# Kernel tuning notes

Hardware: AMD Instinct MI355X
Metric: run time of the kernel (lower is better)

## Reference

```python
import jax, jax.numpy as jnp
import numpy as np

D = 512          # feature dim
N = 4095         # context length
LMBD = 0.9       # eligibility-trace decay
DIM = 2 * D + 1  # 1025
CTX = N + 1      # 4096


def make_M(n: int, lmbd: float) -> jnp.ndarray:
    # M[row, col] = lmbd**(row-col) for col <= row < n, col < n; last row and
    # last column are all zero (M[-1, -1] explicitly zeroed in the original).
    i = jnp.arange(n, dtype=jnp.int32)
    diff = i[:, None] - i[None, :]
    core = jnp.where(diff >= 0, jnp.float32(lmbd) ** jnp.maximum(diff, 0).astype(jnp.float32), 0.0)
    M = jnp.zeros((n + 1, n + 1), dtype=jnp.float32)
    return M.at[:n, :n].set(core)


def setup_inputs() -> dict:
    key = jax.random.key(0)
    kz, kp, kq = jax.random.split(key, 3)
    Z = jax.random.normal(kz, (DIM, CTX), dtype=jnp.float32)
    # nn.Parameter(torch.empty(...)) is uninitialized in the source; use small
    # random values as stand-ins for trained parameters.
    P = jax.random.normal(kp, (DIM, DIM), dtype=jnp.float32) * 0.02
    Q = jax.random.normal(kq, (DIM, DIM), dtype=jnp.float32) * 0.02
    M = make_M(N, LMBD)
    return {"Z": Z, "P": P, "Q": Q, "M": M}


def reference(Z, P, Q, M):
    # X = Z^T Q Z : (CTX, CTX) bilinear attention scores
    X = jnp.einsum("dn,de,em->nm", Z, Q, Z)
    A = jax.nn.softmax(X, axis=-1)          # activation
    # Z + (1/n) * P @ Z @ M @ A ; contract left-to-right to keep (DIM, CTX) intermediates
    PZ = P @ Z                               # (DIM, CTX)
    PZM = PZ @ M                             # (DIM, CTX), M lower-tri decay
    return Z + (1.0 / N) * (PZM @ A)
```

## Files before the change

kernel.cpp:

```cpp
#include <hip/hip_runtime.h>


#define LMBD 0.9f
#define CTXN 4096
#define DIMN 1025
#define DP 1152

#define KSPLIT 1408
#define PSTRIDE ((size_t)DP * CTXN)

typedef __bf16 bf16x8 __attribute__((ext_vector_type(8)));
typedef float f32x4 __attribute__((ext_vector_type(4)));
typedef long lx2 __attribute__((ext_vector_type(2)));

__device__ __forceinline__ unsigned short f2bf(float f) {
  union { float f; unsigned u; } v; v.f = f;
  unsigned r = v.u + 0x7FFFu + ((v.u >> 16) & 1u);
  return (unsigned short)(r >> 16);
}
__device__ __forceinline__ float bf2f(unsigned short h) {
  union { unsigned u; float f; } v; v.u = ((unsigned)h) << 16;
  return v.f;
}

__device__ __forceinline__ void gld_lds16(const void* g, void* l) {
  __builtin_amdgcn_global_load_lds(
      (const __attribute__((address_space(1))) unsigned int*)g,
      (__attribute__((address_space(3))) unsigned int*)l, 16, 0, 0);
}

template <int MODE, int TM, int TN>
__global__ __launch_bounds__(256, 2) void gemm_nt(
    const unsigned short* __restrict__ A, const unsigned short* __restrict__ B,
    void* __restrict__ Cout, int K, int lda, int ldb, int ldc,
    float* __restrict__ pmax, float* __restrict__ psum) {
  constexpr int CA = TM / 16, CB = TN / 16;
  constexpr int FI = TM / 32, FJ = TN / 32;
  __shared__ unsigned short sA[TM * 32];
  __shared__ unsigned short sB[TN * 32];
  const int tid = threadIdx.x;
  const int wave = tid >> 6;
  const int lane = tid & 63;
  const long i0 = (long)blockIdx.x * TM;
  const long j0 = (long)blockIdx.y * TN;
  const int wm = (wave & 1) * (TM / 2);
  const int wn = (wave >> 1) * (TN / 2);

  f32x4 acc[FI][FJ] = {};

  const int srow = lane >> 2;
  const int skc = (((lane & 3) - (lane >> 3)) & 3) * 8;
  const int mrow = lane & 15;
  const int slot = ((((lane >> 4) + (mrow >> 1)) & 3)) * 8;

  for (int k0 = 0; k0 < K; k0 += 32) {
    __syncthreads();
#pragma unroll
    for (int c = 0; c < CA / 4; ++c) {
      const int q = wave * (CA / 4) + c;
      gld_lds16(A + (i0 + q * 16 + srow) * (long)lda + k0 + skc, &sA[q * 512]);
    }
#pragma unroll
    for (int c = 0; c < CB / 4; ++c) {
      const int q = wave * (CB / 4) + c;
      gld_lds16(B + (j0 + q * 16 + srow) * (long)ldb + k0 + skc, &sB[q * 512]);
    }
    __syncthreads();
    bf16x8 af[FI], bfr[FJ];
#pragma unroll
    for (int i = 0; i < FI; ++i)
      af[i] = *(const bf16x8*)&sA[(wm + i * 16 + mrow) * 32 + slot];
#pragma unroll
    for (int j = 0; j < FJ; ++j)
      bfr[j] = *(const bf16x8*)&sB[(wn + j * 16 + mrow) * 32 + slot];
#pragma unroll
    for (int i = 0; i < FI; ++i)
#pragma unroll
      for (int j = 0; j < FJ; ++j)
        acc[i][j] =
            __builtin_amdgcn_mfma_f32_16x16x32_bf16(af[i], bfr[j], acc[i][j], 0, 0, 0);
  }

  const int lr = (lane >> 4) * 4;
  const int lc = lane & 15;
#pragma unroll
  for (int i = 0; i < FI; ++i) {
#pragma unroll
    for (int j = 0; j < FJ; ++j) {
#pragma unroll
      for (int r = 0; r < 4; ++r) {
        const long row = i0 + wm + i * 16 + lr + r;
        const long col = j0 + wn + j * 16 + lc;
        const float v = acc[i][j][r];
        if (MODE == 1) ((float*)Cout)[row * ldc + col] = v;
        else ((unsigned short*)Cout)[row * ldc + col] = f2bf(v);
      }
    }
  }

  if (MODE == 4) {
    float* sMax = (float*)sA;
    float* sSum = (float*)sB;
    const int k8 = (wave & 1) * 4 + (lane >> 4);
    __syncthreads();
#pragma unroll
    for (int j = 0; j < FJ; ++j) {
      float m = -1e30f;
#pragma unroll
      for (int i = 0; i < FI; ++i)
#pragma unroll
        for (int r = 0; r < 4; ++r) m = fmaxf(m, acc[i][j][r]);
      float s = 0.f;
#pragma unroll
      for (int i = 0; i < FI; ++i)
#pragma unroll
        for (int r = 0; r < 4; ++r) s += __expf(acc[i][j][r] - m);
      const int c = wn + j * 16 + lc;
      sMax[c * 8 + k8] = m;
      sSum[c * 8 + k8] = s;
    }
    __syncthreads();
    if (tid < 128) {
      float m = -1e30f;
#pragma unroll
      for (int k = 0; k < 8; ++k) m = fmaxf(m, sMax[tid * 8 + k]);
      float s = 0.f;
#pragma unroll
      for (int k = 0; k < 8; ++k) s += sSum[tid * 8 + k] * __expf(sMax[tid * 8 + k] - m);
      pmax[(size_t)blockIdx.x * CTXN + j0 + tid] = m;
      psum[(size_t)blockIdx.x * CTXN + j0 + tid] = s;
    }
  }
}

__global__ __launch_bounds__(256, 2) void gemm_fp8_splitk(
    const unsigned char* __restrict__ A, const unsigned char* __restrict__ B,
    float* __restrict__ Cout) {
  __shared__ unsigned char sA[128 * 64];
  __shared__ unsigned char sB[128 * 64];
  const int tid = threadIdx.x;
  const int wave = tid >> 6;
  const int lane = tid & 63;
  const unsigned g = blockIdx.x;
  const unsigned bi = g / 96;
  const unsigned rem = g % 96;
  const unsigned bj = rem / 3;
  const unsigned bz = rem % 3;
  const long i0 = (long)bi * 128;
  const long j0 = (long)bj * 128;
  const int wm = (wave & 1) * 64;
  const int wn = (wave >> 1) * 64;
  const int kb = bz * KSPLIT;
  const int ke = min(CTXN, kb + KSPLIT);
  Cout += (size_t)bz * PSTRIDE;

  f32x4 acc[4][4] = {};
  const int srow = lane >> 2;
  const int skc = (((lane & 3) - (lane >> 3)) & 3) * 16;
  const int mrow = lane & 15;
  const int slot = ((((lane >> 4) + (mrow >> 1)) & 3)) * 16;

  for (int k0 = kb; k0 < ke; k0 += 64) {
    __syncthreads();
#pragma unroll
    for (int c = 0; c < 2; ++c) {
      const int q = wave * 2 + c;
      gld_lds16(A + (i0 + q * 16 + srow) * (long)CTXN + k0 + skc, &sA[q * 1024]);
      gld_lds16(B + (j0 + q * 16 + srow) * (long)CTXN + k0 + skc, &sB[q * 1024]);
    }
    __syncthreads();
    lx2 af[4], bfr[4];
#pragma unroll
    for (int i = 0; i < 4; ++i)
      af[i] = *(const lx2*)&sA[(wm + i * 16 + mrow) * 64 + slot];
#pragma unroll
    for (int j = 0; j < 4; ++j)
      bfr[j] = *(const lx2*)&sB[(wn + j * 16 + mrow) * 64 + slot];
#pragma unroll
    for (int i = 0; i < 4; ++i)
#pragma unroll
      for (int j = 0; j < 4; ++j) {
        acc[i][j] = __builtin_amdgcn_mfma_f32_16x16x32_fp8_fp8(af[i].x, bfr[j].x,
                                                               acc[i][j], 0, 0, 0);
        acc[i][j] = __builtin_amdgcn_mfma_f32_16x16x32_fp8_fp8(af[i].y, bfr[j].y,
                                                               acc[i][j], 0, 0, 0);
      }
  }

  const int lr = (lane >> 4) * 4;
  const int lc = lane & 15;
#pragma unroll
  for (int i = 0; i < 4; ++i)
#pragma unroll
    for (int j = 0; j < 4; ++j)
#pragma unroll
      for (int r = 0; r < 4; ++r)
        Cout[(i0 + wm + i * 16 + lr + r) * (long)CTXN + j0 + wn + j * 16 + lc] =
            acc[i][j][r];
}

__global__ void reduce_kernel(const float* __restrict__ Pt, const float* __restrict__ Z,
                              float* __restrict__ out) {
  const size_t idx = ((size_t)blockIdx.x * 256 + threadIdx.x) * 4;
  const f32x4 a = *(const f32x4*)&Pt[idx];
  const f32x4 b = *(const f32x4*)&Pt[PSTRIDE + idx];
  const f32x4 c = *(const f32x4*)&Pt[2 * PSTRIDE + idx];
  const f32x4 z = *(const f32x4*)&Z[idx];
  f32x4 o = z + (a + b + c) * 0.00390625f;
  *(f32x4*)&out[idx] = o;
}

__global__ void pad_kernel(const float* __restrict__ Q, const float* __restrict__ P,
                           unsigned short* __restrict__ Qb,
                           unsigned short* __restrict__ Pb) {
  const int c = blockIdx.x * 128 + threadIdx.x;
  const int r = blockIdx.y;
  const float* src = blockIdx.z ? P : Q;
  unsigned short* dst = blockIdx.z ? Pb : Qb;
  float v = (r < DIMN && c < DIMN) ? src[(size_t)r * DIMN + c] : 0.f;
  dst[(size_t)r * DP + c] = f2bf(v);
}

__global__ void transZ_kernel(const float* __restrict__ Z, unsigned short* __restrict__ ZbT) {
  __shared__ float tile[32][33];
  const int n0 = blockIdx.x * 32, e0 = blockIdx.y * 32;
  const int tx = threadIdx.x, ty = threadIdx.y;
#pragma unroll
  for (int k = 0; k < 4; ++k) {
    const int e = e0 + ty + k * 8;
    tile[ty + k * 8][tx] = (e < DIMN) ? Z[(size_t)e * CTXN + n0 + tx] : 0.f;
  }
  __syncthreads();
#pragma unroll
  for (int k = 0; k < 4; ++k) {
    const int n = n0 + ty + k * 8;
    ZbT[(size_t)n * DP + e0 + tx] = f2bf(tile[tx][ty + k * 8]);
  }
}

__global__ void red2_kernel(const float* __restrict__ pmax, const float* __restrict__ psum,
                            float* __restrict__ rowmax, float* __restrict__ inv_l) {
  const int n = blockIdx.x * 256 + threadIdx.x;
  float M = -1e30f;
  for (int c = 0; c < 32; ++c) M = fmaxf(M, pmax[(size_t)c * CTXN + n]);
  float s = 0.f;
  for (int c = 0; c < 32; ++c)
    s += psum[(size_t)c * CTXN + n] * __expf(pmax[(size_t)c * CTXN + n] - M);
  rowmax[n] = M;
  inv_l[n] = 1.0f / (4095.0f * s);
}

__global__ void ew_kernel(const unsigned short* __restrict__ XT,
                          const float* __restrict__ rowmax, unsigned int* __restrict__ ET) {
  const size_t idx = ((size_t)blockIdx.x * 256 + threadIdx.x) * 4;
  const ushort4 v = *(const ushort4*)&XT[idx];
  const int n = (int)(idx & 4095);
  const float4 rm = *(const float4*)&rowmax[n];
  unsigned p = __builtin_amdgcn_cvt_pk_fp8_f32(__expf(bf2f(v.x) - rm.x),
                                               __expf(bf2f(v.y) - rm.y), 0, false);
  p = __builtin_amdgcn_cvt_pk_fp8_f32(__expf(bf2f(v.z) - rm.z),
                                      __expf(bf2f(v.w) - rm.w), p, true);
  ET[idx >> 2] = p;
}

__global__ __launch_bounds__(256) void scan_kernel(const float* __restrict__ PZ,
                                                   const float* __restrict__ inv_l,
                                                   unsigned char* __restrict__ out) {
  const int d = blockIdx.x;
  const int t = threadIdx.x;
  const float* row = PZ + (size_t)d * CTXN;
  float x[16];
#pragma unroll
  for (int q = 0; q < 4; ++q) {
    const float4 v = *(const float4*)&row[t * 16 + q * 4];
    x[q * 4 + 0] = v.x; x[q * 4 + 1] = v.y; x[q * 4 + 2] = v.z; x[q * 4 + 3] = v.w;
  }
  if (t == 255) x[15] = 0.f;
  float loc[16];
  float run = 0.f;
#pragma unroll
  for (int i = 15; i >= 0; --i) { run = run * LMBD + x[i]; loc[i] = run; }
  __shared__ float sF[256];
  float f = loc[0];
  sF[t] = f;
  __syncthreads();
  float mlt = 0.1853020188851841f;
  for (int step = 1; step < 256; step <<= 1) {
    const float other = (t + step < 256) ? sF[t + step] : 0.f;
    __syncthreads();
    f += mlt * other;
    mlt *= mlt;
    sF[t] = f;
    __syncthreads();
  }
  const float R = (t < 255) ? sF[t + 1] : 0.f;
  float il[16];
#pragma unroll
  for (int q = 0; q < 4; ++q) {
    const float4 v = *(const float4*)&inv_l[t * 16 + q * 4];
    il[q * 4 + 0] = v.x * 256.f; il[q * 4 + 1] = v.y * 256.f;
    il[q * 4 + 2] = v.z * 256.f; il[q * 4 + 3] = v.w * 256.f;
  }
  float o[16];
  float p = 1.f;
#pragma unroll
  for (int i = 15; i >= 0; --i) {
    p *= LMBD;
    o[i] = (loc[i] + p * R) * il[i];
  }
  unsigned w[4];
#pragma unroll
  for (int q = 0; q < 4; ++q) {
    unsigned pk = __builtin_amdgcn_cvt_pk_fp8_f32(o[q * 4 + 0], o[q * 4 + 1], 0, false);
    pk = __builtin_amdgcn_cvt_pk_fp8_f32(o[q * 4 + 2], o[q * 4 + 3], pk, true);
    w[q] = pk;
  }
  *(uint4*)&out[(size_t)d * CTXN + t * 16] = make_uint4(w[0], w[1], w[2], w[3]);
}

extern "C" void kernel_launch(void* const* d_in, const int* in_sizes, int n_in,
                              void* d_out, int out_size, void* d_ws, size_t ws_size,
                              hipStream_t stream) {
  const float* Z = (const float*)d_in[0];
  const float* P = (const float*)d_in[1];
  const float* Q = (const float*)d_in[2];

  char* ws = (char*)d_ws;
  size_t off = 0;
  auto alloc = [&](size_t bytes) {
    void* p = ws + off;
    off += (bytes + 255) & ~(size_t)255;
    return p;
  };
  unsigned char* ET   = (unsigned char*)alloc((size_t)CTXN * CTXN);
  unsigned char* PZMb = (unsigned char*)alloc((size_t)DP * CTXN);
  float* rowmax       = (float*)alloc((size_t)CTXN * 4);
  float* inv_l        = (float*)alloc((size_t)CTXN * 4);
  char* pool = (char*)alloc(0);
  unsigned short* ZbT = (unsigned short*)alloc((size_t)CTXN * DP * 2);
  unsigned short* QZT = (unsigned short*)alloc((size_t)CTXN * DP * 2);
  unsigned short* XT  = (unsigned short*)alloc((size_t)CTXN * CTXN * 2);
  float* PZ           = (float*)alloc((size_t)DP * CTXN * 4);
  unsigned short* Qb  = (unsigned short*)alloc((size_t)DP * DP * 2);
  unsigned short* Pb  = (unsigned short*)alloc((size_t)DP * DP * 2);
  float* pmax         = (float*)alloc((size_t)32 * CTXN * 4);
  float* psum         = (float*)alloc((size_t)32 * CTXN * 4);
  float* partials     = (float*)pool;
  if (off > ws_size) return;

  pad_kernel<<<dim3(9, DP, 2), 128, 0, stream>>>(Q, P, Qb, Pb);
  transZ_kernel<<<dim3(128, 36), dim3(32, 8), 0, stream>>>(Z, ZbT);

  gemm_nt<0, 128, 64><<<dim3(32, 18), 256, 0, stream>>>(ZbT, Qb, QZT, DP, DP, DP, DP,
                                                        nullptr, nullptr);
  gemm_nt<4, 128, 128><<<dim3(32, 32), 256, 0, stream>>>(QZT, ZbT, XT, DP, DP, DP, CTXN,
                                                         pmax, psum);

  red2_kernel<<<16, 256, 0, stream>>>(pmax, psum, rowmax, inv_l);
  ew_kernel<<<16384, 256, 0, stream>>>(XT, rowmax, (unsigned int*)ET);

  gemm_nt<1, 64, 128><<<dim3(18, 32), 256, 0, stream>>>(Pb, ZbT, PZ, DP, DP, DP, CTXN,
                                                        nullptr, nullptr);
  scan_kernel<<<DP, 256, 0, stream>>>(PZ, inv_l, PZMb);

  gemm_fp8_splitk<<<864, 256, 0, stream>>>(PZMb, ET, partials);
  reduce_kernel<<<4100, 256, 0, stream>>>(partials, Z, (float*)d_out);
}
```

Baseline: 286.9 us.

## Merge QZ and PZ GEMMs into one launch, widen split-K with bf16 partials

The QZ and PZ bf16 GEMMs are independent, so they now run as one grid of 1152 blocks dispatched by block index. This fills the GPU better and drops one launch. The final fp8 GEMM raises its split-K factor from 3 to 5 (1440 blocks) for more parallelism and stores the partials as bf16, skipping padded rows, to cut partial-buffer traffic. The reduce kernel sums five bf16 partials. The trade-off is lower precision in the partial sums and more partial reads in the reduce.

New measurement: 274.8 us. -4.2%, faster.

```diff
diff --git a/kernel.cpp b/kernel.cpp
--- a/kernel.cpp
+++ b/kernel.cpp
@@ -6,7 +6,7 @@
 #define DIMN 1025
 #define DP 1152
 
-#define KSPLIT 1408
+#define KSPLIT 832
 #define PSTRIDE ((size_t)DP * CTXN)
 
 typedef __bf16 bf16x8 __attribute__((ext_vector_type(8)));
@@ -30,9 +30,9 @@
 }
 
 template <int MODE, int TM, int TN>
-__global__ __launch_bounds__(256, 2) void gemm_nt(
+__device__ __forceinline__ void gemm_body(
     const unsigned short* __restrict__ A, const unsigned short* __restrict__ B,
-    void* __restrict__ Cout, int K, int lda, int ldb, int ldc,
+    void* __restrict__ Cout, int K, int lda, int ldb, int ldc, int bi, int bj,
     float* __restrict__ pmax, float* __restrict__ psum) {
   constexpr int CA = TM / 16, CB = TN / 16;
   constexpr int FI = TM / 32, FJ = TN / 32;
@@ -41,8 +41,8 @@
   const int tid = threadIdx.x;
   const int wave = tid >> 6;
   const int lane = tid & 63;
-  const long i0 = (long)blockIdx.x * TM;
-  const long j0 = (long)blockIdx.y * TN;
+  const long i0 = (long)bi * TM;
+  const long j0 = (long)bj * TN;
   const int wm = (wave & 1) * (TM / 2);
   const int wn = (wave >> 1) * (TN / 2);
 
@@ -127,25 +127,48 @@
       float s = 0.f;
 #pragma unroll
       for (int k = 0; k < 8; ++k) s += sSum[tid * 8 + k] * __expf(sMax[tid * 8 + k] - m);
-      pmax[(size_t)blockIdx.x * CTXN + j0 + tid] = m;
-      psum[(size_t)blockIdx.x * CTXN + j0 + tid] = s;
-    }
+      pmax[(size_t)bi * CTXN + j0 + tid] = m;
+      psum[(size_t)bi * CTXN + j0 + tid] = s;
+    }
+  }
+}
+
+__global__ __launch_bounds__(256, 2) void gemm_xt(
+    const unsigned short* __restrict__ QZT, const unsigned short* __restrict__ ZbT,
+    unsigned short* __restrict__ XT, float* __restrict__ pmax,
+    float* __restrict__ psum) {
+  gemm_body<4, 128, 128>(QZT, ZbT, XT, DP, DP, DP, CTXN, blockIdx.x, blockIdx.y, pmax,
+                         psum);
+}
+
+__global__ __launch_bounds__(256, 2) void gemm_dual(
+    const unsigned short* __restrict__ ZbT, const unsigned short* __restrict__ Qb,
+    unsigned short* __restrict__ QZT, const unsigned short* __restrict__ Pb,
+    float* __restrict__ PZ) {
+  const unsigned g = blockIdx.x;
+  if (g < 576) {
+    gemm_body<0, 128, 64>(ZbT, Qb, QZT, DP, DP, DP, DP, g & 31, g >> 5, nullptr,
+                          nullptr);
+  } else {
+    const unsigned h = g - 576;
+    gemm_body<1, 64, 128>(Pb, ZbT, PZ, DP, DP, DP, CTXN, h >> 5, h & 31, nullptr,
+                          nullptr);
   }
 }
 
 __global__ __launch_bounds__(256, 2) void gemm_fp8_splitk(
     const unsigned char* __restrict__ A, const unsigned char* __restrict__ B,
-    float* __restrict__ Cout) {
+    unsigned short* __restrict__ Cout) {
   __shared__ unsigned char sA[128 * 64];
   __shared__ unsigned char sB[128 * 64];
   const int tid = threadIdx.x;
   const int wave = tid >> 6;
   const int lane = tid & 63;
   const unsigned g = blockIdx.x;
-  const unsigned bi = g / 96;
-  const unsigned rem = g % 96;
-  const unsigned bj = rem / 3;
-  const unsigned bz = rem % 3;
+  const unsigned bi = g / 160;
+  const unsigned rem = g % 160;
+  const unsigned bj = rem / 5;
+  const unsigned bz = rem % 5;
   const long i0 = (long)bi * 128;
   const long j0 = (long)bj * 128;
   const int wm = (wave & 1) * 64;
@@ -194,19 +217,28 @@
 #pragma unroll
     for (int j = 0; j < 4; ++j)
 #pragma unroll
-      for (int r = 0; r < 4; ++r)
-        Cout[(i0 + wm + i * 16 + lr + r) * (long)CTXN + j0 + wn + j * 16 + lc] =
-            acc[i][j][r];
-}
-
-__global__ void reduce_kernel(const float* __restrict__ Pt, const float* __restrict__ Z,
-                              float* __restrict__ out) {
+      for (int r = 0; r < 4; ++r) {
+        const long row = i0 + wm + i * 16 + lr + r;
+        if (row < DIMN)
+          Cout[row * (long)CTXN + j0 + wn + j * 16 + lc] = f2bf(acc[i][j][r]);
+      }
+}
+
+__global__ void reduce_kernel(const unsigned short* __restrict__ Pt,
+                              const float* __restrict__ Z, float* __restrict__ out) {
   const size_t idx = ((size_t)blockIdx.x * 256 + threadIdx.x) * 4;
-  const f32x4 a = *(const f32x4*)&Pt[idx];
-  const f32x4 b = *(const f32x4*)&Pt[PSTRIDE + idx];
-  const f32x4 c = *(const f32x4*)&Pt[2 * PSTRIDE + idx];
-  const f32x4 z = *(const f32x4*)&Z[idx];
-  f32x4 o = z + (a + b + c) * 0.00390625f;
+  float ax = 0.f, ay = 0.f, az = 0.f, aw = 0.f;
+#pragma unroll
+  for (int z = 0; z < 5; ++z) {
+    const ushort4 v = *(const ushort4*)&Pt[(size_t)z * PSTRIDE + idx];
+    ax += bf2f(v.x); ay += bf2f(v.y); az += bf2f(v.z); aw += bf2f(v.w);
+  }
+  const f32x4 zv = *(const f32x4*)&Z[idx];
+  f32x4 o;
+  o[0] = zv[0] + ax * 0.00390625f;
+  o[1] = zv[1] + ay * 0.00390625f;
+  o[2] = zv[2] + az * 0.00390625f;
+  o[3] = zv[3] + aw * 0.00390625f;
   *(f32x4*)&out[idx] = o;
 }
 
@@ -345,24 +377,21 @@
   unsigned short* Pb  = (unsigned short*)alloc((size_t)DP * DP * 2);
   float* pmax         = (float*)alloc((size_t)32 * CTXN * 4);
   float* psum         = (float*)alloc((size_t)32 * CTXN * 4);
-  float* partials     = (float*)pool;
+  unsigned short* partials = (unsigned short*)pool;
   if (off > ws_size) return;
 
   pad_kernel<<<dim3(9, DP, 2), 128, 0, stream>>>(Q, P, Qb, Pb);
   transZ_kernel<<<dim3(128, 36), dim3(32, 8), 0, stream>>>(Z, ZbT);
 
-  gemm_nt<0, 128, 64><<<dim3(32, 18), 256, 0, stream>>>(ZbT, Qb, QZT, DP, DP, DP, DP,
-                                                        nullptr, nullptr);
-  gemm_nt<4, 128, 128><<<dim3(32, 32), 256, 0, stream>>>(QZT, ZbT, XT, DP, DP, DP, CTXN,
-                                                         pmax, psum);
+  gemm_dual<<<1152, 256, 0, stream>>>(ZbT, Qb, QZT, Pb, PZ);
+
+  gemm_xt<<<dim3(32, 32), 256, 0, stream>>>(QZT, ZbT, XT, pmax, psum);
 
   red2_kernel<<<16, 256, 0, stream>>>(pmax, psum, rowmax, inv_l);
   ew_kernel<<<16384, 256, 0, stream>>>(XT, rowmax, (unsigned int*)ET);
 
-  gemm_nt<1, 64, 128><<<dim3(18, 32), 256, 0, stream>>>(Pb, ZbT, PZ, DP, DP, DP, CTXN,
-                                                        nullptr, nullptr);
   scan_kernel<<<DP, 256, 0, stream>>>(PZ, inv_l, PZMb);
 
-  gemm_fp8_splitk<<<864, 256, 0, stream>>>(PZMb, ET, partials);
+  gemm_fp8_splitk<<<1440, 256, 0, stream>>>(PZMb, ET, partials);
   reduce_kernel<<<4100, 256, 0, stream>>>(partials, Z, (float*)d_out);
 }
```
